# Performance work log

Hardware: AMD Instinct MI355X
Metric: run time of the kernel (lower is better)

Reference implementation:

```python
import jax, jax.numpy as jnp
import numpy as np

S, D, H, HD, CQ, CKV, O = 2048, 2048, 16, 128, 96, 512, 2048


def _linear_params(k, fan_in, fan_out):
    kw, kb = jax.random.split(k)
    lim = 1.0 / np.sqrt(fan_in)
    w = jax.random.uniform(kw, (fan_out, fan_in), minval=-lim, maxval=lim, dtype=jnp.float32)
    b = jax.random.uniform(kb, (fan_out,), minval=-lim, maxval=lim, dtype=jnp.float32)
    return w, b


def setup_inputs() -> dict:
    key = jax.random.key(0)
    ks = jax.random.split(key, 8)
    x = jax.random.normal(ks[0], (S, D), dtype=jnp.float32)
    # standard RoPE tables: theta_i = 10000^(-2i/hd), rotate-half layout
    pos = jnp.arange(S, dtype=jnp.float32)[:, None]              # (S, 1)
    inv_freq = 1.0 / (10000.0 ** (jnp.arange(0, HD, 2, dtype=jnp.float32) / HD))  # (HD/2,)
    ang = pos * inv_freq[None, :]                                 # (S, HD/2)
    rope_cos = jnp.concatenate([jnp.cos(ang), jnp.cos(ang)], axis=-1)  # (S, HD)
    rope_sin = jnp.concatenate([jnp.sin(ang), jnp.sin(ang)], axis=-1)  # (S, HD)
    wq_down, bq_down = _linear_params(ks[1], D, CQ)
    wq_up, bq_up = _linear_params(ks[2], CQ, H * HD)
    wkv_down, bkv_down = _linear_params(ks[3], D, CKV)
    wk_up, bk_up = _linear_params(ks[4], CKV, H * HD)
    wv_up, bv_up = _linear_params(ks[5], CKV, H * HD)
    wo, bo = _linear_params(ks[6], H * HD, O)
    return dict(x=x, rope_cos=rope_cos, rope_sin=rope_sin,
                wq_down=wq_down, bq_down=bq_down, wq_up=wq_up, bq_up=bq_up,
                wkv_down=wkv_down, bkv_down=bkv_down, wk_up=wk_up, bk_up=bk_up,
                wv_up=wv_up, bv_up=bv_up, wo=wo, bo=bo)


def _rope(xh, cos, sin):
    # xh: (S, H, hd); cos/sin: (S, hd) broadcast over heads
    half = xh.shape[-1] // 2
    x1, x2 = xh[..., :half], xh[..., half:]
    rot = jnp.concatenate([-x2, x1], axis=-1)
    return xh * cos[:, None, :] + rot * sin[:, None, :]


def reference(x, rope_cos, rope_sin, wq_down, bq_down, wq_up, bq_up,
              wkv_down, bkv_down, wk_up, bk_up, wv_up, bv_up, wo, bo):
    s = x.shape[0]
    # low-rank Q path: down then up (compressed_q_size < head_dim branch)
    c_q = x @ wq_down.T + bq_down                                  # (S, CQ)
    q = (c_q @ wq_up.T + bq_up).reshape(s, H, HD)                  # (S, H, hd)
    q = _rope(q, rope_cos, rope_sin)
    # shared compressed KV path
    c_kv = x @ wkv_down.T + bkv_down                               # (S, CKV)
    k = _rope((c_kv @ wk_up.T + bk_up).reshape(s, H, HD), rope_cos, rope_sin)
    v = (c_kv @ wv_up.T + bv_up).reshape(s, H, HD)
    # scaled dot-product attention per head (softmax in fp32 as in source)
    q = q / jnp.sqrt(jnp.asarray(HD, q.dtype))
    logits = jnp.einsum('shd,Shd->hsS', q, k)                      # (H, S, S)
    weights = jax.nn.softmax(logits.astype(jnp.float32), axis=-1).astype(logits.dtype)
    attn = jnp.einsum('hsS,Shd->shd', weights, v).reshape(s, H * HD)
    return attn @ wo.T + bo                                        # (S, O)
```

## Files before the change

kernel.cpp:

```cpp
#include <hip/hip_runtime.h>
#include <cstdint>
#include <cstddef>

typedef unsigned short u16;
typedef float f32x4 __attribute__((ext_vector_type(4)));
typedef short s16x8 __attribute__((ext_vector_type(8)));

#define DI __device__ __forceinline__

static constexpr int S_  = 2048;
static constexpr int D_  = 2048;
static constexpr int H_  = 16;
static constexpr int HD_ = 128;
static constexpr int HHD = 2048;
static constexpr int CQP = 128;
static constexpr int NCAT = 640;
static constexpr int CKV_ = 512;
static constexpr float QSCALE = 0.12751743360294163f;

DI u16 f2bf(float f) {
  unsigned u = __float_as_uint(f);
  u += 0x7fffu + ((u >> 16) & 1u);
  return (u16)(u >> 16);
}
DI float bf2f(u16 h) { return __uint_as_float(((unsigned)h) << 16); }

DI void store_c(float* C, long long i, float v) { C[i] = v; }
DI void store_c(u16* C, long long i, float v) { C[i] = f2bf(v); }

template <int CTRL>
DI float dppf(float x) {
  return __uint_as_float((unsigned)__builtin_amdgcn_mov_dpp(
      (int)__float_as_uint(x), CTRL, 0xf, 0xf, true));
}
DI float red_max16(float x) {
  x = fmaxf(x, dppf<0xB1>(x));
  x = fmaxf(x, dppf<0x4E>(x));
  x = fmaxf(x, dppf<0x141>(x));
  x = fmaxf(x, dppf<0x140>(x));
  return x;
}
DI float red_sum16(float x) {
  x += dppf<0xB1>(x);
  x += dppf<0x4E>(x);
  x += dppf<0x141>(x);
  x += dppf<0x140>(x);
  return x;
}

#define GLD16(g, l)                                                        \
  __builtin_amdgcn_global_load_lds(                                        \
      (__attribute__((address_space(1))) void*)(void*)(const void*)(g),    \
      (__attribute__((address_space(3))) void*)(l), 16, 0, 0)

template <typename OutT, int BCOL, int BROW, int BN>
DI void gemm_core(u16* __restrict__ Asm, u16* __restrict__ Bsm,
                  const u16* __restrict__ A, const u16* __restrict__ B,
                  OutT* __restrict__ C,
                  const float* __restrict__ bias_col,
                  const float* __restrict__ bias_row,
                  int K, int lda, int ldb, int ldc) {
  constexpr int MI = (BN == 128) ? 4 : 2;
  constexpr int NI = 4;
  constexpr int NCH = 8 + BN / 16;
  constexpr int NC4 = NCH / 4;
  const int tid  = threadIdx.x;
  const int w    = tid >> 6;
  const int lane = tid & 63;
  const int lr   = lane & 15;
  const int lq   = lane >> 4;
  const long long m0 = (long long)blockIdx.y * 128;
  const long long n0 = (long long)blockIdx.x * BN;
  const int wr = (BN == 128) ? (w >> 1) * 64 : w * 32;
  const int wc = (BN == 128) ? (w & 1) * 64 : 0;

  f32x4 acc[MI][NI];
#pragma unroll
  for (int i = 0; i < MI; ++i)
#pragma unroll
    for (int j = 0; j < NI; ++j)
#pragma unroll
      for (int r = 0; r < 4; ++r) acc[i][j][r] = 0.f;

  const int rch = lane >> 2, cch = (lane & 3) * 8;
  const u16* gsrc[NC4];
  u16* ldst[NC4];
  int bstep[NC4];
#pragma unroll
  for (int ci = 0; ci < NC4; ++ci) {
    const int c = w + ci * 4;
    if (c < 8) {
      gsrc[ci] = A + (m0 + c * 16 + rch) * lda + cch;
      ldst[ci] = &Asm[c * 512];
      bstep[ci] = 128 * 32;
    } else {
      gsrc[ci] = B + (n0 + (c - 8) * 16 + rch) * ldb + cch;
      ldst[ci] = &Bsm[(c - 8) * 512];
      bstep[ci] = BN * 32;
    }
  }
  auto stage = [&](int kt, int b) {
#pragma unroll
    for (int ci = 0; ci < NC4; ++ci) GLD16(gsrc[ci] + kt, ldst[ci] + b * bstep[ci]);
  };

  stage(0, 0);
  int cur = 0;
  for (int kt = 0; kt < K; kt += 32) {
    __syncthreads();
    if (kt + 32 < K) stage(kt + 32, cur ^ 1);
    const u16* Ab = &Asm[cur * 128 * 32];
    const u16* Bb = &Bsm[cur * BN * 32];

    s16x8 af[MI], bfr[NI];
#pragma unroll
    for (int tm = 0; tm < MI; ++tm)
      af[tm] = *(const s16x8*)&Ab[(wr + tm * 16 + lr) * 32 + lq * 8];
#pragma unroll
    for (int tn = 0; tn < NI; ++tn)
      bfr[tn] = *(const s16x8*)&Bb[(wc + tn * 16 + lr) * 32 + lq * 8];
#pragma unroll
    for (int tm = 0; tm < MI; ++tm)
#pragma unroll
      for (int tn = 0; tn < NI; ++tn)
        acc[tm][tn] = __builtin_amdgcn_mfma_f32_16x16x32_bf16(af[tm], bfr[tn],
                                                              acc[tm][tn], 0, 0, 0);
    cur ^= 1;
  }

#pragma unroll
  for (int tm = 0; tm < MI; ++tm)
#pragma unroll
    for (int tn = 0; tn < NI; ++tn) {
      const long long col = n0 + wc + tn * 16 + lr;
      float bc = BCOL ? bias_col[col] : 0.f;
#pragma unroll
      for (int r = 0; r < 4; ++r) {
        const long long row = m0 + wr + tm * 16 + lq * 4 + r;
        float v = acc[tm][tn][r] + bc;
        if (BROW) v += bias_row[row];
        store_c(C, row * (long long)ldc + col, v);
      }
    }
}

template <typename OutT, int BCOL, int BROW, int BN>
__global__ __launch_bounds__(256) void gemm_bt(
    const u16* __restrict__ A, const u16* __restrict__ B, OutT* __restrict__ C,
    const float* __restrict__ bias_col, const float* __restrict__ bias_row,
    int K, int lda, int ldb, int ldc,
    long long sA, long long sB, long long sC) {
  __shared__ __align__(16) u16 As[2 * 128 * 32];
  __shared__ __align__(16) u16 Bs[2 * BN * 32];
  gemm_core<OutT, BCOL, BROW, BN>(
      As, Bs, A + (long long)blockIdx.z * sA, B + (long long)blockIdx.z * sB,
      C + (long long)blockIdx.z * sC, bias_col, bias_row, K, lda, ldb, ldc);
}

__global__ __launch_bounds__(256, 3) void up3(
    const u16* __restrict__ ccat, const u16* __restrict__ wqu,
    const u16* __restrict__ wku, const u16* __restrict__ wvu,
    const float* __restrict__ bq_up, const float* __restrict__ bk_up,
    const float* __restrict__ bv_up,
    u16* __restrict__ qb, u16* __restrict__ kb, u16* __restrict__ vT) {
  __shared__ __align__(16) u16 As[2 * 128 * 32];
  __shared__ __align__(16) u16 Bs[2 * 128 * 32];
  if (blockIdx.z == 0)
    gemm_core<u16, 1, 0, 128>(As, Bs, ccat, wqu, qb, bq_up, nullptr,
                              CQP, NCAT, CQP, HHD);
  else if (blockIdx.z == 1)
    gemm_core<u16, 1, 0, 128>(As, Bs, ccat + CQP, wku, kb, bk_up, nullptr,
                              CKV_, NCAT, CKV_, HHD);
  else
    gemm_core<u16, 0, 1, 128>(As, Bs, wvu, ccat + CQP, vT, nullptr, bv_up,
                              CKV_, CKV_, NCAT, S_);
}

DI void store4(float* d, long long e, float4 s) { *(float4*)(d + e) = s; }
DI void store4(u16* d, long long e, float4 s) {
  unsigned lo = (unsigned)f2bf(s.x) | ((unsigned)f2bf(s.y) << 16);
  unsigned hi = (unsigned)f2bf(s.z) | ((unsigned)f2bf(s.w) << 16);
  *(uint2*)(d + e) = make_uint2(lo, hi);
}
template <typename OutT>
__global__ __launch_bounds__(256) void combine_z(
    const float* __restrict__ p, long long zs, int nz,
    const float* __restrict__ bias, OutT* __restrict__ dst, int ldc, int n4) {
  int i = blockIdx.x * 256 + threadIdx.x;
  if (i >= n4) return;
  long long e = (long long)i * 4;
  float4 s = *(const float4*)(p + e);
  for (int z = 1; z < nz; ++z) {
    float4 t = *(const float4*)(p + (long long)z * zs + e);
    s.x += t.x; s.y += t.y; s.z += t.z; s.w += t.w;
  }
  int c = (int)(e % ldc);
  s.x += bias[c]; s.y += bias[c + 1]; s.z += bias[c + 2]; s.w += bias[c + 3];
  store4(dst, e, s);
}

__global__ __launch_bounds__(256, 2) void flash_attn(
    const u16* __restrict__ Q, const u16* __restrict__ Kg,
    const u16* __restrict__ Vt, float* __restrict__ Op, float* __restrict__ ml) {
  __shared__ __align__(16) u16 Ks[128 * 128];
  __shared__ __align__(16) u16 Vs[128 * 128];
  const int h = blockIdx.x;
  const int t = blockIdx.y;
  const int kspl = blockIdx.z;
  const int tid = threadIdx.x;
  const int w = tid >> 6, lane = tid & 63, lr = lane & 15, lq = lane >> 4;
  const int qg = t * 128 + w * 32;
  const int tr = tid >> 4;
  const int csw = (tid & 15) ^ (tr & 7);

  s16x8 qf[2][4];
#pragma unroll
  for (int mi = 0; mi < 2; ++mi)
#pragma unroll
    for (int kst = 0; kst < 4; ++kst)
      qf[mi][kst] = *(const s16x8*)&Q[(size_t)(qg + mi * 16 + lr) * HHD +
                                      h * HD_ + kst * 32 + lq * 8];

  f32x4 oacc[2][8];
  float m[2][4], l[2][4];
#pragma unroll
  for (int mi = 0; mi < 2; ++mi) {
#pragma unroll
    for (int r = 0; r < 4; ++r) { m[mi][r] = -1.0e38f; l[mi][r] = 0.f; }
#pragma unroll
    for (int f = 0; f < 8; ++f)
#pragma unroll
      for (int r = 0; r < 4; ++r) oacc[mi][f][r] = 0.f;
  }

  auto stage_k = [&](int j) {
    const u16* s0 = Kg + (size_t)(j * 128 + tr) * HHD + h * HD_ + csw * 8;
#pragma unroll
    for (int i = 0; i < 8; ++i)
      GLD16(s0 + (size_t)i * 16 * HHD, &Ks[i * 2048 + w * 512]);
  };
  auto stage_v = [&](int j) {
    const u16* s0 = Vt + (size_t)(h * HD_ + tr) * S_ + j * 128 + csw * 8;
#pragma unroll
    for (int i = 0; i < 8; ++i)
      GLD16(s0 + (size_t)i * 16 * S_, &Vs[i * 2048 + w * 512]);
  };

  const int j0 = kspl * 8;
  stage_k(j0);
  stage_v(j0);

  for (int jj = 0; jj < 8; ++jj) {
    __syncthreads();

    f32x4 sacc[2][8];
#pragma unroll
    for (int mi = 0; mi < 2; ++mi)
#pragma unroll
      for (int f = 0; f < 8; ++f)
#pragma unroll
        for (int r = 0; r < 4; ++r) sacc[mi][f][r] = 0.f;
#pragma unroll
    for (int kst = 0; kst < 4; ++kst)
#pragma unroll
      for (int f = 0; f < 8; ++f) {
        s16x8 kf = *(const s16x8*)
            &Ks[(f * 16 + lr) * 128 + (((kst * 4 + lq) ^ (lr & 7)) << 3)];
        sacc[0][f] = __builtin_amdgcn_mfma_f32_16x16x32_bf16(qf[0][kst], kf,
                                                             sacc[0][f], 0, 0, 0);
        sacc[1][f] = __builtin_amdgcn_mfma_f32_16x16x32_bf16(qf[1][kst], kf,
                                                             sacc[1][f], 0, 0, 0);
      }

#pragma unroll
    for (int mi = 0; mi < 2; ++mi)
#pragma unroll
      for (int r = 0; r < 4; ++r) {
        float mx = sacc[mi][0][r];
#pragma unroll
        for (int f = 1; f < 8; ++f) mx = fmaxf(mx, sacc[mi][f][r]);
        mx = red_max16(mx);
        float mn = fmaxf(m[mi][r], mx);
        float al = exp2f(m[mi][r] - mn);
        m[mi][r] = mn;
        float sum = 0.f;
#pragma unroll
        for (int f = 0; f < 8; ++f) {
          float p = exp2f(sacc[mi][f][r] - mn);
          sacc[mi][f][r] = p;
          sum += p;
        }
        sum = red_sum16(sum);
        l[mi][r] = l[mi][r] * al + sum;
#pragma unroll
        for (int f = 0; f < 8; ++f) oacc[mi][f][r] *= al;
      }

    __syncthreads();

#pragma unroll
    for (int mi = 0; mi < 2; ++mi)
#pragma unroll
      for (int r = 0; r < 4; ++r) {
        const int q = w * 32 + mi * 16 + lq * 4 + r;
#pragma unroll
        for (int f = 0; f < 8; ++f) {
          const int ch = (2 * f + (lr >> 3)) ^ (q & 7);
          Ks[q * 128 + ch * 8 + (lr & 7)] = f2bf(sacc[mi][f][r]);
        }
      }

    __syncthreads();

#pragma unroll
    for (int kst = 0; kst < 4; ++kst) {
      s16x8 pa0 = *(const s16x8*)
          &Ks[(w * 32 + lr) * 128 + (((kst * 4 + lq) ^ (lr & 7)) << 3)];
      s16x8 pa1 = *(const s16x8*)
          &Ks[(w * 32 + 16 + lr) * 128 + (((kst * 4 + lq) ^ (lr & 7)) << 3)];
#pragma unroll
      for (int f = 0; f < 8; ++f) {
        s16x8 vf = *(const s16x8*)
            &Vs[(f * 16 + lr) * 128 + (((kst * 4 + lq) ^ (lr & 7)) << 3)];
        oacc[0][f] = __builtin_amdgcn_mfma_f32_16x16x32_bf16(pa0, vf,
                                                             oacc[0][f], 0, 0, 0);
        oacc[1][f] = __builtin_amdgcn_mfma_f32_16x16x32_bf16(pa1, vf,
                                                             oacc[1][f], 0, 0, 0);
      }
    }

    __syncthreads();
    if (jj < 7) {
      stage_k(j0 + jj + 1);
      stage_v(j0 + jj + 1);
    }
  }

#pragma unroll
  for (int mi = 0; mi < 2; ++mi) {
#pragma unroll
    for (int r = 0; r < 4; ++r) {
      const int row = qg + mi * 16 + lq * 4 + r;
      if (lr == 0) {
        float* p = &ml[((size_t)(kspl * S_ + row) * H_ + h) * 2];
        p[0] = m[mi][r];
        p[1] = l[mi][r];
      }
#pragma unroll
      for (int f = 0; f < 8; ++f)
        Op[(size_t)(kspl * S_ + row) * HHD + h * HD_ + f * 16 + lr] =
            oacc[mi][f][r];
    }
  }
}

__global__ __launch_bounds__(256) void flash_combine(
    const float* __restrict__ Op, const float* __restrict__ ml,
    u16* __restrict__ attnb) {
  int i = blockIdx.x * 256 + threadIdx.x;
  long long e = (long long)i * 4;
  int s = (int)(e >> 11);
  int h = ((int)e & 2047) >> 7;
  const float* p0 = &ml[((size_t)s * H_ + h) * 2];
  const float* p1 = &ml[((size_t)(S_ + s) * H_ + h) * 2];
  float m0 = p0[0], l0 = p0[1], m1 = p1[0], l1 = p1[1];
  float M = fmaxf(m0, m1);
  float w0 = exp2f(m0 - M), w1 = exp2f(m1 - M);
  float inv = 1.f / (w0 * l0 + w1 * l1);
  float4 a = *(const float4*)&Op[e];
  float4 b = *(const float4*)&Op[(size_t)S_ * HHD + e];
  float4 o;
  o.x = (w0 * a.x + w1 * b.x) * inv;
  o.y = (w0 * a.y + w1 * b.y) * inv;
  o.z = (w0 * a.z + w1 * b.z) * inv;
  o.w = (w0 * a.w + w1 * b.w) * inv;
  unsigned lo = (unsigned)f2bf(o.x) | ((unsigned)f2bf(o.y) << 16);
  unsigned hi = (unsigned)f2bf(o.z) | ((unsigned)f2bf(o.w) << 16);
  *(uint2*)(attnb + e) = make_uint2(lo, hi);
}

DI void cast4(const float* __restrict__ s, u16* __restrict__ d, int v) {
  float4 f = ((const float4*)s)[v];
  unsigned lo = (unsigned)f2bf(f.x) | ((unsigned)f2bf(f.y) << 16);
  unsigned hi = (unsigned)f2bf(f.z) | ((unsigned)f2bf(f.w) << 16);
  ((uint2*)d)[v] = make_uint2(lo, hi);
}
DI void store_bf4(u16* __restrict__ d, long long i, float4 f) {
  unsigned lo = (unsigned)f2bf(f.x) | ((unsigned)f2bf(f.y) << 16);
  unsigned hi = (unsigned)f2bf(f.z) | ((unsigned)f2bf(f.w) << 16);
  *(uint2*)(d + i) = make_uint2(lo, hi);
}
static constexpr int PV_XB   = 1048576;
static constexpr int PV_WCAT = 327680;
static constexpr int PV_WQU  = 65536;
static constexpr int PV_WKU  = 262144;
static constexpr int PV_WVU  = 262144;
static constexpr int PV_WOB  = 1048576;
static constexpr int PV_BCAT = 160;
static constexpr int PV_TOT  = PV_XB + PV_WCAT + PV_WQU + PV_WKU + PV_WVU + PV_WOB + PV_BCAT;

__global__ __launch_bounds__(256) void prep(
    const float* __restrict__ x, const float* __restrict__ wqd_s,
    const float* __restrict__ wkvd_s, const float* __restrict__ wqu_s,
    const float* __restrict__ wku_s, const float* __restrict__ wvu_s,
    const float* __restrict__ wo_s, const float* __restrict__ bqd_s,
    const float* __restrict__ bkvd_s,
    u16* __restrict__ xb, u16* __restrict__ wcat, u16* __restrict__ wqu,
    u16* __restrict__ wku, u16* __restrict__ wvu, u16* __restrict__ wob,
    float* __restrict__ bcat) {
  int v = blockIdx.x * 256 + threadIdx.x;
  if (v >= PV_TOT) return;
  if (v < PV_XB) { cast4(x, xb, v); return; }
  v -= PV_XB;
  if (v < PV_WCAT) {
    int i = v * 4, n = i >> 11, k = i & 2047;
    float4 o = make_float4(0.f, 0.f, 0.f, 0.f);
    if (n < 96)        o = *(const float4*)&wqd_s[n * D_ + k];
    else if (n >= 128) o = *(const float4*)&wkvd_s[(n - 128) * D_ + k];
    store_bf4(wcat, i, o);
    return;
  }
  v -= PV_WCAT;
  if (v < PV_WQU) {
    int i = v * 4, r = i >> 7, c = i & 127;
    float4 o = (c < 96) ? *(const float4*)&wqu_s[r * 96 + c]
                        : make_float4(0.f, 0.f, 0.f, 0.f);
    store_bf4(wqu, i, o);
    return;
  }
  v -= PV_WQU;
  if (v < PV_WKU) { cast4(wku_s, wku, v); return; }
  v -= PV_WKU;
  if (v < PV_WVU) { cast4(wvu_s, wvu, v); return; }
  v -= PV_WVU;
  if (v < PV_WOB) { cast4(wo_s, wob, v); return; }
  v -= PV_WOB;
  {
    int i = v * 4;
    float4 o;
    float* po = &o.x;
#pragma unroll
    for (int jj = 0; jj < 4; ++jj) {
      int e = i + jj;
      po[jj] = (e < 96) ? bqd_s[e] : (e < 128 ? 0.f : bkvd_s[e - 128]);
    }
    *(float4*)&bcat[i] = o;
  }
}

__global__ __launch_bounds__(256) void rope2(u16* __restrict__ qb,
                                             u16* __restrict__ kb,
                                             const float* __restrict__ cs,
                                             const float* __restrict__ sn) {
  int id = blockIdx.x * 256 + threadIdx.x;
  const bool isq = id < S_ * H_ * 64;
  if (!isq) id -= S_ * H_ * 64;
  u16* X = isq ? qb : kb;
  const float scale = isq ? QSCALE : 1.0f;
  int d = id & 63;
  int h = (id >> 6) & 15;
  int s = id >> 10;
  long long b = (long long)s * HHD + h * HD_ + d;
  float x1 = bf2f(X[b]), x2 = bf2f(X[b + 64]);
  int cb = s * HD_ + d;
  float o1 = (x1 * cs[cb] - x2 * sn[cb]) * scale;
  float o2 = (x2 * cs[cb + 64] + x1 * sn[cb + 64]) * scale;
  X[b] = f2bf(o1);
  X[b + 64] = f2bf(o2);
}

extern "C" void kernel_launch(void* const* d_in, const int* in_sizes, int n_in,
                              void* d_out, int out_size, void* d_ws, size_t ws_size,
                              hipStream_t stream) {
  (void)in_sizes; (void)n_in; (void)out_size; (void)ws_size;
  const float* x        = (const float*)d_in[0];
  const float* rc       = (const float*)d_in[1];
  const float* rs       = (const float*)d_in[2];
  const float* wq_down  = (const float*)d_in[3];
  const float* bq_down  = (const float*)d_in[4];
  const float* wq_up    = (const float*)d_in[5];
  const float* bq_up    = (const float*)d_in[6];
  const float* wkv_down = (const float*)d_in[7];
  const float* bkv_down = (const float*)d_in[8];
  const float* wk_up    = (const float*)d_in[9];
  const float* bk_up    = (const float*)d_in[10];
  const float* wv_up    = (const float*)d_in[11];
  const float* bv_up    = (const float*)d_in[12];
  const float* wo       = (const float*)d_in[13];
  const float* bo       = (const float*)d_in[14];
  float* out = (float*)d_out;

  char* ws = (char*)d_ws;
  size_t off = 0;
  auto alloc = [&](size_t bytes) -> void* {
    off = (off + 255) & ~(size_t)255;
    void* p = ws + off;
    off += bytes;
    return p;
  };

  u16* xb      = (u16*)alloc((size_t)S_ * D_ * 2);
  u16* wcat    = (u16*)alloc((size_t)NCAT * D_ * 2);
  float* bcat  = (float*)alloc(NCAT * 4);
  u16* wqu     = (u16*)alloc((size_t)HHD * CQP * 2);
  u16* wku     = (u16*)alloc((size_t)HHD * CKV_ * 2);
  u16* wvu     = (u16*)alloc((size_t)HHD * CKV_ * 2);
  u16* wob     = (u16*)alloc((size_t)D_ * HHD * 2);
  u16* ccat    = (u16*)alloc((size_t)S_ * NCAT * 2);
  u16* qb      = (u16*)alloc((size_t)S_ * HHD * 2);
  u16* kb      = (u16*)alloc((size_t)S_ * HHD * 2);
  u16* vT      = (u16*)alloc((size_t)HHD * S_ * 2);
  u16* attnb   = (u16*)alloc((size_t)S_ * HHD * 2);
  float* Op    = (float*)alloc((size_t)2 * S_ * HHD * 4);
  float* ml    = (float*)alloc((size_t)2 * S_ * H_ * 2 * 4);
  float* pool  = (float*)alloc((size_t)2 * S_ * D_ * 4);
  float* pcat  = pool;
  float* pout  = pool;

  prep<<<(PV_TOT + 255) / 256, 256, 0, stream>>>(
      x, wq_down, wkv_down, wq_up, wk_up, wv_up, wo, bq_down, bkv_down,
      xb, wcat, wqu, wku, wvu, wob, bcat);

  gemm_bt<float, 0, 0, 64><<<dim3(NCAT / 64, 16, 4), 256, 0, stream>>>(
      xb, wcat, pcat, nullptr, nullptr, 512, D_, D_, NCAT,
      512, 512, (long long)S_ * NCAT);
  combine_z<u16><<<(S_ * NCAT / 4 + 255) / 256, 256, 0, stream>>>(
      pcat, (long long)S_ * NCAT, 4, bcat, ccat, NCAT, S_ * NCAT / 4);

  up3<<<dim3(16, 16, 3), 256, 0, stream>>>(
      ccat, wqu, wku, wvu, bq_up, bk_up, bv_up, qb, kb, vT);

  rope2<<<(2 * S_ * H_ * 64) / 256, 256, 0, stream>>>(qb, kb, rc, rs);

  flash_attn<<<dim3(H_, S_ / 128, 2), 256, 0, stream>>>(qb, kb, vT, Op, ml);
  flash_combine<<<(S_ * HHD / 4) / 256, 256, 0, stream>>>(Op, ml, attnb);

  gemm_bt<float, 0, 0, 128><<<dim3(16, 16, 2), 256, 0, stream>>>(
      attnb, wob, pout, nullptr, nullptr, 1024, HHD, HHD, D_,
      1024, 1024, (long long)S_ * D_);
  combine_z<float><<<(S_ * D_ / 4 + 255) / 256, 256, 0, stream>>>(
      pout, (long long)S_ * D_, 2, bo, out, D_, S_ * D_ / 4);
}
```

Baseline: 329.9 us.

## Split keys across warp pairs inside flash block and fuse split-K combine

The flash attention kernel drops the grid-level key split. Each block now handles 64 queries with two warp groups, each owning half of every 128-key tile. The partial outputs are merged in shared memory and written directly as bf16, which removes the fp32 Op/ml buffers and the separate flash_combine kernel. P gets its own shared buffer so the next K tile can be staged right after the P write, and V staging is deferred to the end of the iteration. This costs an extra 16KB of LDS per block and a larger per-block reduction epilogue.

Result: faster. 272.4 us (-17.4%).

```diff
diff --git a/kernel.cpp b/kernel.cpp
--- a/kernel.cpp
+++ b/kernel.cpp
@@ -201,15 +201,17 @@
 
 __global__ __launch_bounds__(256, 2) void flash_attn(
     const u16* __restrict__ Q, const u16* __restrict__ Kg,
-    const u16* __restrict__ Vt, float* __restrict__ Op, float* __restrict__ ml) {
+    const u16* __restrict__ Vt, u16* __restrict__ Og) {
   __shared__ __align__(16) u16 Ks[128 * 128];
   __shared__ __align__(16) u16 Vs[128 * 128];
+  __shared__ __align__(16) u16 Ps[64 * 128];
   const int h = blockIdx.x;
   const int t = blockIdx.y;
-  const int kspl = blockIdx.z;
   const int tid = threadIdx.x;
   const int w = tid >> 6, lane = tid & 63, lr = lane & 15, lq = lane >> 4;
-  const int qg = t * 128 + w * 32;
+  const int g = w >> 1;
+  const int wq = w & 1;
+  const int qw = t * 64 + wq * 32;
   const int tr = tid >> 4;
   const int csw = (tid & 15) ^ (tr & 7);
 
@@ -218,7 +220,7 @@
   for (int mi = 0; mi < 2; ++mi)
 #pragma unroll
     for (int kst = 0; kst < 4; ++kst)
-      qf[mi][kst] = *(const s16x8*)&Q[(size_t)(qg + mi * 16 + lr) * HHD +
+      qf[mi][kst] = *(const s16x8*)&Q[(size_t)(qw + mi * 16 + lr) * HHD +
                                       h * HD_ + kst * 32 + lq * 8];
 
   f32x4 oacc[2][8];
@@ -246,26 +248,25 @@
       GLD16(s0 + (size_t)i * 16 * S_, &Vs[i * 2048 + w * 512]);
   };
 
-  const int j0 = kspl * 8;
-  stage_k(j0);
-  stage_v(j0);
-
-  for (int jj = 0; jj < 8; ++jj) {
-    __syncthreads();
-
-    f32x4 sacc[2][8];
+  stage_k(0);
+  stage_v(0);
+  __syncthreads();
+
+  for (int j = 0; j < 16; ++j) {
+    f32x4 sacc[2][4];
 #pragma unroll
     for (int mi = 0; mi < 2; ++mi)
 #pragma unroll
-      for (int f = 0; f < 8; ++f)
+      for (int f = 0; f < 4; ++f)
 #pragma unroll
         for (int r = 0; r < 4; ++r) sacc[mi][f][r] = 0.f;
 #pragma unroll
     for (int kst = 0; kst < 4; ++kst)
 #pragma unroll
-      for (int f = 0; f < 8; ++f) {
+      for (int f = 0; f < 4; ++f) {
+        const int key = g * 64 + f * 16 + lr;
         s16x8 kf = *(const s16x8*)
-            &Ks[(f * 16 + lr) * 128 + (((kst * 4 + lq) ^ (lr & 7)) << 3)];
+            &Ks[key * 128 + (((kst * 4 + lq) ^ (key & 7)) << 3)];
         sacc[0][f] = __builtin_amdgcn_mfma_f32_16x16x32_bf16(qf[0][kst], kf,
                                                              sacc[0][f], 0, 0, 0);
         sacc[1][f] = __builtin_amdgcn_mfma_f32_16x16x32_bf16(qf[1][kst], kf,
@@ -278,14 +279,14 @@
       for (int r = 0; r < 4; ++r) {
         float mx = sacc[mi][0][r];
 #pragma unroll
-        for (int f = 1; f < 8; ++f) mx = fmaxf(mx, sacc[mi][f][r]);
+        for (int f = 1; f < 4; ++f) mx = fmaxf(mx, sacc[mi][f][r]);
         mx = red_max16(mx);
         float mn = fmaxf(m[mi][r], mx);
         float al = exp2f(m[mi][r] - mn);
         m[mi][r] = mn;
         float sum = 0.f;
 #pragma unroll
-        for (int f = 0; f < 8; ++f) {
+        for (int f = 0; f < 4; ++f) {
           float p = exp2f(sacc[mi][f][r] - mn);
           sacc[mi][f][r] = p;
           sum += p;
@@ -296,32 +297,31 @@
         for (int f = 0; f < 8; ++f) oacc[mi][f][r] *= al;
       }
 
+#pragma unroll
+    for (int mi = 0; mi < 2; ++mi)
+#pragma unroll
+      for (int r = 0; r < 4; ++r) {
+        const int q = wq * 32 + mi * 16 + lq * 4 + r;
+#pragma unroll
+        for (int f = 0; f < 4; ++f) {
+          const int ch = (g * 8 + f * 2 + (lr >> 3)) ^ (q & 7);
+          Ps[q * 128 + ch * 8 + (lr & 7)] = f2bf(sacc[mi][f][r]);
+        }
+      }
+
     __syncthreads();
-
-#pragma unroll
-    for (int mi = 0; mi < 2; ++mi)
-#pragma unroll
-      for (int r = 0; r < 4; ++r) {
-        const int q = w * 32 + mi * 16 + lq * 4 + r;
-#pragma unroll
-        for (int f = 0; f < 8; ++f) {
-          const int ch = (2 * f + (lr >> 3)) ^ (q & 7);
-          Ks[q * 128 + ch * 8 + (lr & 7)] = f2bf(sacc[mi][f][r]);
-        }
-      }
-
-    __syncthreads();
-
-#pragma unroll
-    for (int kst = 0; kst < 4; ++kst) {
-      s16x8 pa0 = *(const s16x8*)
-          &Ks[(w * 32 + lr) * 128 + (((kst * 4 + lq) ^ (lr & 7)) << 3)];
-      s16x8 pa1 = *(const s16x8*)
-          &Ks[(w * 32 + 16 + lr) * 128 + (((kst * 4 + lq) ^ (lr & 7)) << 3)];
+    if (j < 15) stage_k(j + 1);
+
+#pragma unroll
+    for (int kst = 0; kst < 2; ++kst) {
+      const int chA = (g * 8 + kst * 4 + lq) ^ (lr & 7);
+      s16x8 pa0 = *(const s16x8*)&Ps[(wq * 32 + lr) * 128 + chA * 8];
+      s16x8 pa1 = *(const s16x8*)&Ps[(wq * 32 + 16 + lr) * 128 + chA * 8];
 #pragma unroll
       for (int f = 0; f < 8; ++f) {
+        const int d = f * 16 + lr;
         s16x8 vf = *(const s16x8*)
-            &Vs[(f * 16 + lr) * 128 + (((kst * 4 + lq) ^ (lr & 7)) << 3)];
+            &Vs[d * 128 + (((g * 8 + kst * 4 + lq) ^ (d & 7)) << 3)];
         oacc[0][f] = __builtin_amdgcn_mfma_f32_16x16x32_bf16(pa0, vf,
                                                              oacc[0][f], 0, 0, 0);
         oacc[1][f] = __builtin_amdgcn_mfma_f32_16x16x32_bf16(pa1, vf,
@@ -330,53 +330,42 @@
     }
 
     __syncthreads();
-    if (jj < 7) {
-      stage_k(j0 + jj + 1);
-      stage_v(j0 + jj + 1);
-    }
-  }
-
-#pragma unroll
-  for (int mi = 0; mi < 2; ++mi) {
-#pragma unroll
-    for (int r = 0; r < 4; ++r) {
-      const int row = qg + mi * 16 + lq * 4 + r;
-      if (lr == 0) {
-        float* p = &ml[((size_t)(kspl * S_ + row) * H_ + h) * 2];
-        p[0] = m[mi][r];
-        p[1] = l[mi][r];
-      }
-#pragma unroll
-      for (int f = 0; f < 8; ++f)
-        Op[(size_t)(kspl * S_ + row) * HHD + h * HD_ + f * 16 + lr] =
-            oacc[mi][f][r];
-    }
-  }
-}
-
-__global__ __launch_bounds__(256) void flash_combine(
-    const float* __restrict__ Op, const float* __restrict__ ml,
-    u16* __restrict__ attnb) {
-  int i = blockIdx.x * 256 + threadIdx.x;
-  long long e = (long long)i * 4;
-  int s = (int)(e >> 11);
-  int h = ((int)e & 2047) >> 7;
-  const float* p0 = &ml[((size_t)s * H_ + h) * 2];
-  const float* p1 = &ml[((size_t)(S_ + s) * H_ + h) * 2];
-  float m0 = p0[0], l0 = p0[1], m1 = p1[0], l1 = p1[1];
-  float M = fmaxf(m0, m1);
-  float w0 = exp2f(m0 - M), w1 = exp2f(m1 - M);
-  float inv = 1.f / (w0 * l0 + w1 * l1);
-  float4 a = *(const float4*)&Op[e];
-  float4 b = *(const float4*)&Op[(size_t)S_ * HHD + e];
-  float4 o;
-  o.x = (w0 * a.x + w1 * b.x) * inv;
-  o.y = (w0 * a.y + w1 * b.y) * inv;
-  o.z = (w0 * a.z + w1 * b.z) * inv;
-  o.w = (w0 * a.w + w1 * b.w) * inv;
-  unsigned lo = (unsigned)f2bf(o.x) | ((unsigned)f2bf(o.y) << 16);
-  unsigned hi = (unsigned)f2bf(o.z) | ((unsigned)f2bf(o.w) << 16);
-  *(uint2*)(attnb + e) = make_uint2(lo, hi);
+    if (j < 15) stage_v(j + 1);
+  }
+
+  float* KsF = (float*)Ks;
+  float* mlF = (float*)Ps;
+  if (g == 1) {
+#pragma unroll
+    for (int mi = 0; mi < 2; ++mi)
+#pragma unroll
+      for (int r = 0; r < 4; ++r) {
+        const int q = wq * 32 + mi * 16 + lq * 4 + r;
+        if (lr == 0) { mlF[q * 2] = m[mi][r]; mlF[q * 2 + 1] = l[mi][r]; }
+#pragma unroll
+        for (int f = 0; f < 8; ++f)
+          KsF[q * 128 + f * 16 + lr] = oacc[mi][f][r];
+      }
+  }
+  __syncthreads();
+  if (g == 0) {
+#pragma unroll
+    for (int mi = 0; mi < 2; ++mi)
+#pragma unroll
+      for (int r = 0; r < 4; ++r) {
+        const int q = wq * 32 + mi * 16 + lq * 4 + r;
+        float m1 = mlF[q * 2], l1 = mlF[q * 2 + 1];
+        float M = fmaxf(m[mi][r], m1);
+        float w0 = exp2f(m[mi][r] - M), w1 = exp2f(m1 - M);
+        float inv = 1.f / (w0 * l[mi][r] + w1 * l1);
+        w0 *= inv; w1 *= inv;
+#pragma unroll
+        for (int f = 0; f < 8; ++f) {
+          float o = w0 * oacc[mi][f][r] + w1 * KsF[q * 128 + f * 16 + lr];
+          Og[(size_t)(t * 64 + q) * HHD + h * HD_ + f * 16 + lr] = f2bf(o);
+        }
+      }
+  }
 }
 
 DI void cast4(const float* __restrict__ s, u16* __restrict__ d, int v) {
@@ -511,8 +500,6 @@
   u16* kb      = (u16*)alloc((size_t)S_ * HHD * 2);
   u16* vT      = (u16*)alloc((size_t)HHD * S_ * 2);
   u16* attnb   = (u16*)alloc((size_t)S_ * HHD * 2);
-  float* Op    = (float*)alloc((size_t)2 * S_ * HHD * 4);
-  float* ml    = (float*)alloc((size_t)2 * S_ * H_ * 2 * 4);
   float* pool  = (float*)alloc((size_t)2 * S_ * D_ * 4);
   float* pcat  = pool;
   float* pout  = pool;
@@ -532,8 +519,7 @@
 
   rope2<<<(2 * S_ * H_ * 64) / 256, 256, 0, stream>>>(qb, kb, rc, rs);
 
-  flash_attn<<<dim3(H_, S_ / 128, 2), 256, 0, stream>>>(qb, kb, vT, Op, ml);
-  flash_combine<<<(S_ * HHD / 4) / 256, 256, 0, stream>>>(Op, ml, attnb);
+  flash_attn<<<dim3(H_, S_ / 64, 1), 256, 0, stream>>>(qb, kb, vT, attnb);
 
   gemm_bt<float, 0, 0, 128><<<dim3(16, 16, 2), 256, 0, stream>>>(
       attnb, wob, pout, nullptr, nullptr, 1024, HHD, HHD, D_,
```
